# Performance work log

Measured on AMD Instinct MI355X. Metric: run time of the kernel, lower is better.

## Reference

```python
import jax, jax.numpy as jnp
import numpy as np

DIM = 1024
DIM_MEDIA = 1024
DIM_HEAD = 64
HEADS = 8
INNER = DIM_HEAD * HEADS  # 512
B, N_TOK, N_LAT = 4, 4096, 1024
LN_EPS = 1e-5


def setup_inputs() -> dict:
    key = jax.random.key(0)
    ks = jax.random.split(key, 6)
    x = jax.random.normal(ks[0], (B, N_TOK, DIM), dtype=jnp.float32)
    media = jax.random.normal(ks[1], (B, N_LAT, DIM_MEDIA), dtype=jnp.float32)
    media_mask = jax.random.randint(ks[2], (B, N_LAT), 0, 2).astype(bool)
    media_mask = media_mask.at[:, 0].set(True)  # avoid fully-masked rows (NaN softmax)
    ln_gamma = jnp.ones((DIM,), jnp.float32)
    ln_beta = jnp.zeros((DIM,), jnp.float32)
    Wq = jax.random.normal(ks[3], (DIM, INNER), jnp.float32) * (DIM ** -0.5)
    Wkv = jax.random.normal(ks[4], (DIM_MEDIA, 2 * INNER), jnp.float32) * (DIM_MEDIA ** -0.5)
    Wout = jax.random.normal(ks[5], (INNER, DIM), jnp.float32) * (INNER ** -0.5)
    return {"x": x, "media": media, "media_mask": media_mask,
            "ln_gamma": ln_gamma, "ln_beta": ln_beta,
            "Wq": Wq, "Wkv": Wkv, "Wout": Wout}


def reference(x, media, media_mask, ln_gamma, ln_beta, Wq, Wkv, Wout):
    scale = DIM_HEAD ** -0.5
    # LayerNorm over last dim
    mu = jnp.mean(x, axis=-1, keepdims=True)
    var = jnp.mean(jnp.square(x - mu), axis=-1, keepdims=True)
    xn = (x - mu) * jax.lax.rsqrt(var + LN_EPS) * ln_gamma + ln_beta

    q = (xn @ Wq) * scale                      # [b, n, inner]
    kv = media @ Wkv                           # [b, m, 2*inner]
    k, v = jnp.split(kv, 2, axis=-1)

    def to_heads(t):
        b, n, _ = t.shape
        return t.reshape(b, n, HEADS, DIM_HEAD).transpose(0, 2, 1, 3)  # b h n d

    q, k, v = to_heads(q), to_heads(k), to_heads(v)

    sim = jnp.einsum('bhid,bhjd->bhij', q, k)  # [b, h, n_tok, n_lat]
    neg_inf = jnp.float32(-jnp.inf)
    sim = jnp.where(media_mask[:, None, None, :], sim, neg_inf)
    sim = sim - jax.lax.stop_gradient(jnp.max(sim, axis=-1, keepdims=True))
    attn = jax.nn.softmax(sim, axis=-1)
    out = jnp.einsum('bhij,bhjd->bhid', attn, v)  # [b, h, n_tok, d]
    out = out.transpose(0, 2, 1, 3).reshape(out.shape[0], out.shape[2], INNER)
    return out @ Wout  # [b, n_tok, dim]
```

## Files before the change

### kernel.cpp

```cpp
#include <hip/hip_runtime.h>
#include <hip/hip_bf16.h>

typedef short bf16x8 __attribute__((ext_vector_type(8)));
typedef float f32x4 __attribute__((ext_vector_type(4)));
typedef unsigned short u16;

#define AS1 __attribute__((address_space(1)))
#define AS3 __attribute__((address_space(3)))

#define DIM     1024
#define INNER   512
#define HEADS   8
#define DHEAD   64
#define BATCH   4
#define NTOK    4096
#define NLAT    1024
#define M_X     (BATCH*NTOK)
#define M_MED   (BATCH*NLAT)
#define LN_EPS  1e-5f

__device__ __forceinline__ float b2f(u16 h) {
    union { unsigned u; float f; } v; v.u = ((unsigned)h) << 16; return v.f;
}
__device__ __forceinline__ u16 f2b(float f) {
    union { float f; unsigned u; } v; v.f = f;
    unsigned r = v.u + 0x7fff + ((v.u >> 16) & 1);
    return (u16)(r >> 16);
}

__launch_bounds__(256)
__global__ void detect_kernel(const unsigned* __restrict__ xw, const unsigned* __restrict__ maskw,
                              unsigned* __restrict__ flags) {
    __shared__ int s_bad, s_byte;
    if (threadIdx.x == 0) { s_bad = 0; s_byte = 0; }
    __syncthreads();
    unsigned w = xw[threadIdx.x];
    int bad = 0;
    #pragma unroll
    for (int h = 0; h < 2; h++) {
        unsigned el = (h ? (w >> 16) : w) & 0xFFFFu;
        unsigned ef = (el >> 7) & 0xFFu;
        if (!((ef >= 64u && ef < 192u) || (el & 0x7FFFu) == 0u)) bad = 1;
    }
    if (bad) atomicOr(&s_bad, 1);
    for (int i = threadIdx.x; i < NLAT; i += 256)
        if (maskw[i] > 1u) { atomicOr(&s_byte, 1); break; }
    __syncthreads();
    if (threadIdx.x == 0) { flags[0] = s_bad ? 0u : 1u; flags[1] = s_byte ? 1u : 0u; }
}

#define PREP_BLOCKS 8196

__device__ __forceinline__ void do_transpose(const void* in, u16* out, int R, int C,
                                             int bx, int by, bool bf, u16 (*t)[33]) {
    int c0 = bx * 32, r0 = by * 32;
    int tid = threadIdx.x;
    int r = tid >> 3, cb = (tid & 7) * 4;
    size_t base = (size_t)(r0 + r) * C + c0 + cb;
    u16 e0, e1, e2, e3;
    if (bf) {
        ushort4 a = *(const ushort4*)((const u16*)in + base);
        e0 = a.x; e1 = a.y; e2 = a.z; e3 = a.w;
    } else {
        float4 a = *(const float4*)((const float*)in + base);
        e0 = f2b(a.x); e1 = f2b(a.y); e2 = f2b(a.z); e3 = f2b(a.w);
    }
    t[r][cb] = e0; t[r][cb + 1] = e1; t[r][cb + 2] = e2; t[r][cb + 3] = e3;
    __syncthreads();
    ushort4 o;
    o.x = t[cb + 0][r]; o.y = t[cb + 1][r]; o.z = t[cb + 2][r]; o.w = t[cb + 3][r];
    *(ushort4*)(out + (size_t)(c0 + r) * R + r0 + cb) = o;
}

__launch_bounds__(256)
__global__ void prep_kernel(const void* __restrict__ x, const void* __restrict__ g,
                            const void* __restrict__ bt, u16* __restrict__ xn,
                            const void* __restrict__ media, u16* __restrict__ media_c,
                            const void* __restrict__ mask, int* __restrict__ map,
                            int* __restrict__ cnt,
                            const void* __restrict__ Wq, u16* __restrict__ WqT,
                            const void* __restrict__ Wkv, u16* __restrict__ WkvT,
                            const void* __restrict__ Wout, u16* __restrict__ WoutT,
                            const unsigned* __restrict__ flags) {
    __shared__ int wsumI[4];
    __shared__ u16 t[32][33];
    bool bf = flags[0] != 0;
    int bid = blockIdx.x, tid = threadIdx.x;

    if (bid < 4096) {
        int w = tid >> 6, lane = tid & 63;
        int row = (bid << 2) + w;
        float v[16];
        if (bf) {
            const u16* xr = (const u16*)x + (size_t)row * DIM;
            #pragma unroll
            for (int i = 0; i < 2; i++) {
                bf16x8 a = *(const bf16x8*)(xr + (size_t)(lane + 64 * i) * 8);
                #pragma unroll
                for (int j = 0; j < 8; j++) v[i * 8 + j] = b2f((u16)a[j]);
            }
        } else {
            const float* xr = (const float*)x + (size_t)row * DIM;
            #pragma unroll
            for (int i = 0; i < 4; i++) {
                float4 a = *(const float4*)(xr + (size_t)(lane + 64 * i) * 4);
                v[i * 4 + 0] = a.x; v[i * 4 + 1] = a.y;
                v[i * 4 + 2] = a.z; v[i * 4 + 3] = a.w;
            }
        }
        float s = 0.f, s2 = 0.f;
        #pragma unroll
        for (int i = 0; i < 16; i++) { s += v[i]; s2 += v[i] * v[i]; }
        #pragma unroll
        for (int m = 1; m < 64; m <<= 1) { s += __shfl_xor(s, m); s2 += __shfl_xor(s2, m); }
        float mu = s * (1.f / DIM);
        float var = s2 * (1.f / DIM) - mu * mu;
        float inv = rsqrtf(fmaxf(var, 0.f) + LN_EPS);
        u16* orow = xn + (size_t)row * DIM;
        if (bf) {
            const u16* gr = (const u16*)g;
            const u16* br = (const u16*)bt;
            #pragma unroll
            for (int i = 0; i < 2; i++) {
                int c = (lane + 64 * i) * 8;
                bf16x8 ga = *(const bf16x8*)(gr + c);
                bf16x8 ba = *(const bf16x8*)(br + c);
                u16 o[8];
                #pragma unroll
                for (int j = 0; j < 8; j++)
                    o[j] = f2b((v[i * 8 + j] - mu) * inv * b2f((u16)ga[j]) + b2f((u16)ba[j]));
                *(bf16x8*)(orow + c) = *(bf16x8*)o;
            }
        } else {
            const float* gr = (const float*)g;
            const float* br = (const float*)bt;
            #pragma unroll
            for (int i = 0; i < 4; i++) {
                int c = (lane + 64 * i) * 4;
                float4 ga = *(const float4*)(gr + c);
                float4 ba = *(const float4*)(br + c);
                ushort4 o;
                o.x = f2b((v[i * 4 + 0] - mu) * inv * ga.x + ba.x);
                o.y = f2b((v[i * 4 + 1] - mu) * inv * ga.y + ba.y);
                o.z = f2b((v[i * 4 + 2] - mu) * inv * ga.z + ba.z);
                o.w = f2b((v[i * 4 + 3] - mu) * inv * ga.w + ba.w);
                *(ushort4*)(orow + c) = o;
            }
        }
    } else if (bid < 6144) {
        size_t i = ((size_t)(bid - 4096) * 256 + tid) * 8;
        if (bf) {
            *(bf16x8*)(media_c + i) = *(const bf16x8*)((const u16*)media + i);
        } else {
            const float* s = (const float*)media + i;
            float4 a = *(const float4*)s, b = *(const float4*)(s + 4);
            u16 o[8] = {f2b(a.x), f2b(a.y), f2b(a.z), f2b(a.w),
                        f2b(b.x), f2b(b.y), f2b(b.z), f2b(b.w)};
            *(bf16x8*)(media_c + i) = *(bf16x8*)o;
        }
    } else if (bid < 6148) {
        int b = bid - 6144;
        bool bytes = flags[1] != 0;
        int v[4];
        if (bytes) {
            unsigned wd = ((const unsigned*)mask)[b * 256 + tid];
            #pragma unroll
            for (int i = 0; i < 4; i++) v[i] = ((wd >> (8 * i)) & 0xFFu) ? 1 : 0;
        } else {
            int4 m4 = ((const int4*)mask)[b * 256 + tid];
            v[0] = m4.x != 0; v[1] = m4.y != 0; v[2] = m4.z != 0; v[3] = m4.w != 0;
        }
        int tsum = v[0] + v[1] + v[2] + v[3];
        int lane = tid & 63, w = tid >> 6;
        int incl = tsum;
        #pragma unroll
        for (int off = 1; off < 64; off <<= 1) {
            int tt = __shfl_up(incl, off);
            if (lane >= off) incl += tt;
        }
        if (lane == 63) wsumI[w] = incl;
        __syncthreads();
        int base = 0;
        for (int k = 0; k < w; k++) base += wsumI[k];
        int slot = base + incl - tsum;
        int gbase = b * NLAT + tid * 4;
        #pragma unroll
        for (int i = 0; i < 4; i++) map[gbase + i] = v[i] ? slot++ : -1;
        if (tid == 0) cnt[b] = wsumI[0] + wsumI[1] + wsumI[2] + wsumI[3];
    } else if (bid < 6660) {
        int idx = bid - 6148;
        do_transpose(Wq, WqT, DIM, INNER, idx & 15, idx >> 4, bf, t);
    } else if (bid < 7684) {
        int idx = bid - 6660;
        do_transpose(Wkv, WkvT, DIM, DIM, idx & 31, idx >> 5, bf, t);
    } else {
        int idx = bid - 7684;
        do_transpose(Wout, WoutT, INNER, DIM, idx & 31, idx >> 5, bf, t);
    }
}

__launch_bounds__(256, 2)
__global__ void gemm128(const u16* __restrict__ A, const u16* __restrict__ Bt,
                        u16* __restrict__ C, float* __restrict__ Cf, int Ndim, int K,
                        float scale, int mode, u16* __restrict__ vT,
                        const int* __restrict__ map,
                        const unsigned* __restrict__ flags) {
    __shared__ __align__(16) u16 As[128 * 32];
    __shared__ __align__(16) u16 Bs[128 * 32];
    bool outbf = (mode != 2) || (flags[0] != 0);
    int n0 = blockIdx.x * 128, m0 = blockIdx.y * 128;
    int tid = threadIdx.x;
    int w = tid >> 6, lane = tid & 63, quad = lane >> 4, l15 = lane & 15;
    int wm = (w >> 1) * 64, wn = (w & 1) * 64;
    f32x4 acc[4][4] = {};
    int rowInSeg = lane >> 2;
    int colB = (((lane & 3) ^ ((lane >> 3) & 3))) * 8;
    for (int k0 = 0; k0 < K; k0 += 32) {
        __syncthreads();
        #pragma unroll
        for (int i = 0; i < 2; i++) {
            int seg = w * 2 + i;
            int row = seg * 16 + rowInSeg;
            __builtin_amdgcn_global_load_lds(
                (const AS1 void*)(A + (size_t)(m0 + row) * K + k0 + colB),
                (AS3 void*)(As + seg * 512), 16, 0, 0);
            __builtin_amdgcn_global_load_lds(
                (const AS1 void*)(Bt + (size_t)(n0 + row) * K + k0 + colB),
                (AS3 void*)(Bs + seg * 512), 16, 0, 0);
        }
        __syncthreads();
        int sw = quad ^ ((l15 >> 1) & 3);
        bf16x8 af[4], bfr[4];
        #pragma unroll
        for (int i = 0; i < 4; i++)
            af[i] = *(bf16x8*)&As[(wm + i * 16 + l15) * 32 + sw * 8];
        #pragma unroll
        for (int j = 0; j < 4; j++)
            bfr[j] = *(bf16x8*)&Bs[(wn + j * 16 + l15) * 32 + sw * 8];
        #pragma unroll
        for (int i = 0; i < 4; i++)
            #pragma unroll
            for (int j = 0; j < 4; j++)
                acc[i][j] = __builtin_amdgcn_mfma_f32_16x16x32_bf16(af[i], bfr[j], acc[i][j], 0, 0, 0);
    }
    #pragma unroll
    for (int i = 0; i < 4; i++)
        #pragma unroll
        for (int j = 0; j < 4; j++)
            #pragma unroll
            for (int r = 0; r < 4; r++) {
                int row = m0 + wm + i * 16 + quad * 4 + r;
                int col = n0 + wn + j * 16 + l15;
                float val = acc[i][j][r] * scale;
                if (mode == 1) {
                    int b = row >> 10, jj = row & 1023;
                    int slot = map[(b << 10) + jj];
                    if (slot >= 0) {
                        if (col < INNER) {
                            C[((size_t)(b << 10) + slot) * INNER + col] = f2b(val);
                        } else {
                            int c = col - INNER;
                            int h = c >> 6, d = c & 63;
                            vT[(((size_t)(b * HEADS + h) * 64 + d) << 10) + slot] = f2b(val);
                        }
                    }
                } else if (outbf) {
                    C[(size_t)row * Ndim + col] = f2b(val);
                } else {
                    Cf[(size_t)row * Ndim + col] = val;
                }
            }
}

__launch_bounds__(256, 6)
__global__ void flash_kernel(const u16* __restrict__ q, const u16* __restrict__ Kc,
                             const u16* __restrict__ vTc, const int* __restrict__ cntp,
                             u16* __restrict__ attn_out) {
    __shared__ __align__(16) u16 Ks[64 * 64];
    __shared__ __align__(16) u16 Vts[64 * 64];
    __shared__ __align__(16) u16 Ps[4][16 * 68];
    int bh = blockIdx.x >> 6;
    int qt = blockIdx.x & 63;
    int b = bh >> 3, h = bh & 7;
    int tid = threadIdx.x, w = tid >> 6, lane = tid & 63, quad = lane >> 4, l15 = lane & 15;
    int qrow0 = qt * 64 + w * 16;
    int cnt = cntp[b];

    size_t qbase = ((size_t)(b * NTOK) + qrow0 + l15) * INNER + h * 64;
    bf16x8 qf[2];
    qf[0] = *(const bf16x8*)(q + qbase + quad * 8);
    qf[1] = *(const bf16x8*)(q + qbase + 32 + quad * 8);

    f32x4 Oacc[4] = {};
    float lsum[4] = {0.f, 0.f, 0.f, 0.f};
    int ld_row = lane >> 3;
    int ld_col = ((lane & 7) ^ ld_row) * 8;

    for (int jt = 0; jt < cnt; jt += 64) {
        __syncthreads();
        #pragma unroll
        for (int i = 0; i < 2; i++) {
            int seg = w * 2 + i;
            int j = jt + seg * 8 + ld_row;
            __builtin_amdgcn_global_load_lds(
                (const AS1 void*)(Kc + ((size_t)(b * NLAT) + j) * INNER + h * 64 + ld_col),
                (AS3 void*)(Ks + seg * 512), 16, 0, 0);
            int d = seg * 8 + ld_row;
            __builtin_amdgcn_global_load_lds(
                (const AS1 void*)(vTc + (((size_t)(b * HEADS + h) * 64 + d) << 10) + jt + ld_col),
                (AS3 void*)(Vts + seg * 512), 16, 0, 0);
        }
        __syncthreads();

        int sw0 = (quad ^ (l15 & 7)) * 8;
        int sw1 = ((quad + 4) ^ (l15 & 7)) * 8;
        f32x4 S[4];
        #pragma unroll
        for (int c = 0; c < 4; c++) {
            bf16x8 kf0 = *(bf16x8*)&Ks[(c * 16 + l15) * 64 + sw0];
            bf16x8 kf1 = *(bf16x8*)&Ks[(c * 16 + l15) * 64 + sw1];
            f32x4 s = {};
            s = __builtin_amdgcn_mfma_f32_16x16x32_bf16(qf[0], kf0, s, 0, 0, 0);
            s = __builtin_amdgcn_mfma_f32_16x16x32_bf16(qf[1], kf1, s, 0, 0, 0);
            S[c] = s;
        }
        #pragma unroll
        for (int c = 0; c < 4; c++) {
            bool valid = (jt + c * 16 + l15) < cnt;
            #pragma unroll
            for (int r = 0; r < 4; r++) {
                float p = valid ? __expf(fminf(S[c][r], 80.f)) : 0.f;
                lsum[r] += p;
                Ps[w][(quad * 4 + r) * 68 + c * 16 + l15] = f2b(p);
            }
        }
        asm volatile("s_waitcnt lgkmcnt(0)" ::: "memory");
        bf16x8 pf0 = *(bf16x8*)&Ps[w][l15 * 68 + quad * 8];
        bf16x8 pf1 = *(bf16x8*)&Ps[w][l15 * 68 + 32 + quad * 8];
        #pragma unroll
        for (int dt = 0; dt < 4; dt++) {
            bf16x8 vf0 = *(bf16x8*)&Vts[(dt * 16 + l15) * 64 + sw0];
            bf16x8 vf1 = *(bf16x8*)&Vts[(dt * 16 + l15) * 64 + sw1];
            Oacc[dt] = __builtin_amdgcn_mfma_f32_16x16x32_bf16(pf0, vf0, Oacc[dt], 0, 0, 0);
            Oacc[dt] = __builtin_amdgcn_mfma_f32_16x16x32_bf16(pf1, vf1, Oacc[dt], 0, 0, 0);
        }
    }
    #pragma unroll
    for (int r = 0; r < 4; r++) {
        float l = lsum[r];
        l += __shfl_xor(l, 1);
        l += __shfl_xor(l, 2);
        l += __shfl_xor(l, 4);
        l += __shfl_xor(l, 8);
        float invl = (l > 0.f) ? (1.f / l) : 0.f;
        #pragma unroll
        for (int dt = 0; dt < 4; dt++) {
            int row = qrow0 + quad * 4 + r;
            int col = h * 64 + dt * 16 + l15;
            attn_out[(size_t)(b * NTOK + row) * INNER + col] = f2b(Oacc[dt][r] * invl);
        }
    }
}

extern "C" void kernel_launch(void* const* d_in, const int* in_sizes, int n_in,
                              void* d_out, int out_size, void* d_ws, size_t ws_size,
                              hipStream_t stream) {
    const void* x     = d_in[0];
    const void* media = d_in[1];
    const void* mask  = d_in[2];
    const void* g     = d_in[3];
    const void* beta  = d_in[4];
    const void* Wq    = d_in[5];
    const void* Wkv   = d_in[6];
    const void* Wout  = d_in[7];

    char* ws = (char*)d_ws;
    unsigned* flags = (unsigned*)ws;   ws += 256;
    int* map_c  = (int*)ws;            ws += (size_t)M_MED * 4;
    int* cnt_c  = (int*)ws;            ws += 256;
    u16* media_c = (u16*)ws;           ws += (size_t)M_MED * DIM * 2;
    u16* xn    = (u16*)ws;             ws += (size_t)M_X * DIM * 2;
    u16* qb    = (u16*)ws;             ws += (size_t)M_X * INNER * 2;
    u16* Kb    = (u16*)ws;             ws += (size_t)M_MED * INNER * 2;
    u16* vTb   = (u16*)ws;             ws += (size_t)M_MED * INNER * 2;
    u16* ao    = (u16*)ws;             ws += (size_t)M_X * INNER * 2;
    u16* WqT   = (u16*)ws;             ws += (size_t)DIM * INNER * 2;
    u16* WkvT  = (u16*)ws;             ws += (size_t)DIM * DIM * 2;
    u16* WoutT = (u16*)ws;             ws += (size_t)INNER * DIM * 2;

    detect_kernel<<<1, 256, 0, stream>>>((const unsigned*)x, (const unsigned*)mask, flags);
    prep_kernel<<<PREP_BLOCKS, 256, 0, stream>>>(x, g, beta, xn, media, media_c, mask, map_c, cnt_c,
                                                 Wq, WqT, Wkv, WkvT, Wout, WoutT, flags);
    gemm128<<<dim3(INNER / 128, M_X / 128), 256, 0, stream>>>(xn, WqT, qb, (float*)nullptr, INNER, DIM,
                                                              0.125f, 0, (u16*)nullptr, (int*)nullptr, flags);
    gemm128<<<dim3(DIM / 128, M_MED / 128), 256, 0, stream>>>(media_c, WkvT, Kb, (float*)nullptr, DIM, DIM,
                                                              1.0f, 1, vTb, map_c, flags);
    flash_kernel<<<dim3(32 * 64), 256, 0, stream>>>(qb, Kb, vTb, cnt_c, ao);
    gemm128<<<dim3(DIM / 128, M_X / 128), 256, 0, stream>>>(ao, WoutT, (u16*)d_out, (float*)d_out, DIM, INNER,
                                                            1.0f, 2, (u16*)nullptr, (int*)nullptr, flags);
}
```

Measured before the change: 288.7 us.

## Double-buffer LDS tiles in GEMM and flash attention kernels

Both the GEMM and the flash attention kernel now keep two LDS buffers and issue the global-to-LDS load for the next K/V or K-slice tile before computing on the current one. This removes one barrier per iteration and lets memory latency overlap the MFMA work. In exchange LDS use per block doubles and the launch bounds change (GEMM from 2 to 3 blocks per CU, flash from 6 to 3), which alters occupancy. In the flash kernel the Ps writes and the final vmcnt wait now share iterations with in-flight prefetches.

```diff
diff --git a/kernel.cpp b/kernel.cpp
--- a/kernel.cpp
+++ b/kernel.cpp
@@ -199,14 +199,14 @@
     }
 }
 
-__launch_bounds__(256, 2)
+__launch_bounds__(256, 3)
 __global__ void gemm128(const u16* __restrict__ A, const u16* __restrict__ Bt,
                         u16* __restrict__ C, float* __restrict__ Cf, int Ndim, int K,
                         float scale, int mode, u16* __restrict__ vT,
                         const int* __restrict__ map,
                         const unsigned* __restrict__ flags) {
-    __shared__ __align__(16) u16 As[128 * 32];
-    __shared__ __align__(16) u16 Bs[128 * 32];
+    __shared__ __align__(16) u16 As[2][128 * 32];
+    __shared__ __align__(16) u16 Bs[2][128 * 32];
     bool outbf = (mode != 2) || (flags[0] != 0);
     int n0 = blockIdx.x * 128, m0 = blockIdx.y * 128;
     int tid = threadIdx.x;
@@ -215,33 +215,44 @@
     f32x4 acc[4][4] = {};
     int rowInSeg = lane >> 2;
     int colB = (((lane & 3) ^ ((lane >> 3) & 3))) * 8;
-    for (int k0 = 0; k0 < K; k0 += 32) {
-        __syncthreads();
+    int sw = quad ^ ((l15 >> 1) & 3);
+
+    auto STAGE = [&](int buf, int k0) {
         #pragma unroll
         for (int i = 0; i < 2; i++) {
             int seg = w * 2 + i;
             int row = seg * 16 + rowInSeg;
             __builtin_amdgcn_global_load_lds(
                 (const AS1 void*)(A + (size_t)(m0 + row) * K + k0 + colB),
-                (AS3 void*)(As + seg * 512), 16, 0, 0);
+                (AS3 void*)(&As[buf][seg * 512]), 16, 0, 0);
             __builtin_amdgcn_global_load_lds(
                 (const AS1 void*)(Bt + (size_t)(n0 + row) * K + k0 + colB),
-                (AS3 void*)(Bs + seg * 512), 16, 0, 0);
-        }
-        __syncthreads();
-        int sw = quad ^ ((l15 >> 1) & 3);
+                (AS3 void*)(&Bs[buf][seg * 512]), 16, 0, 0);
+        }
+    };
+
+    int nt = K >> 5;
+    STAGE(0, 0);
+    asm volatile("s_waitcnt vmcnt(0)" ::: "memory");
+    __syncthreads();
+    int cur = 0;
+    for (int t = 0; t < nt; ++t) {
+        if (t + 1 < nt) STAGE(cur ^ 1, (t + 1) << 5);
         bf16x8 af[4], bfr[4];
         #pragma unroll
         for (int i = 0; i < 4; i++)
-            af[i] = *(bf16x8*)&As[(wm + i * 16 + l15) * 32 + sw * 8];
+            af[i] = *(bf16x8*)&As[cur][(wm + i * 16 + l15) * 32 + sw * 8];
         #pragma unroll
         for (int j = 0; j < 4; j++)
-            bfr[j] = *(bf16x8*)&Bs[(wn + j * 16 + l15) * 32 + sw * 8];
+            bfr[j] = *(bf16x8*)&Bs[cur][(wn + j * 16 + l15) * 32 + sw * 8];
         #pragma unroll
         for (int i = 0; i < 4; i++)
             #pragma unroll
             for (int j = 0; j < 4; j++)
                 acc[i][j] = __builtin_amdgcn_mfma_f32_16x16x32_bf16(af[i], bfr[j], acc[i][j], 0, 0, 0);
+        asm volatile("s_waitcnt vmcnt(0)" ::: "memory");
+        __syncthreads();
+        cur ^= 1;
     }
     #pragma unroll
     for (int i = 0; i < 4; i++)
@@ -272,12 +283,12 @@
             }
 }
 
-__launch_bounds__(256, 6)
+__launch_bounds__(256, 3)
 __global__ void flash_kernel(const u16* __restrict__ q, const u16* __restrict__ Kc,
                              const u16* __restrict__ vTc, const int* __restrict__ cntp,
                              u16* __restrict__ attn_out) {
-    __shared__ __align__(16) u16 Ks[64 * 64];
-    __shared__ __align__(16) u16 Vts[64 * 64];
+    __shared__ __align__(16) u16 Ks[2][64 * 64];
+    __shared__ __align__(16) u16 Vts[2][64 * 64];
     __shared__ __align__(16) u16 Ps[4][16 * 68];
     int bh = blockIdx.x >> 6;
     int qt = blockIdx.x & 63;
@@ -296,29 +307,36 @@
     int ld_row = lane >> 3;
     int ld_col = ((lane & 7) ^ ld_row) * 8;
 
-    for (int jt = 0; jt < cnt; jt += 64) {
-        __syncthreads();
+    auto STAGE = [&](int buf, int jt) {
         #pragma unroll
         for (int i = 0; i < 2; i++) {
             int seg = w * 2 + i;
             int j = jt + seg * 8 + ld_row;
             __builtin_amdgcn_global_load_lds(
                 (const AS1 void*)(Kc + ((size_t)(b * NLAT) + j) * INNER + h * 64 + ld_col),
-                (AS3 void*)(Ks + seg * 512), 16, 0, 0);
+                (AS3 void*)(&Ks[buf][seg * 512]), 16, 0, 0);
             int d = seg * 8 + ld_row;
             __builtin_amdgcn_global_load_lds(
                 (const AS1 void*)(vTc + (((size_t)(b * HEADS + h) * 64 + d) << 10) + jt + ld_col),
-                (AS3 void*)(Vts + seg * 512), 16, 0, 0);
-        }
-        __syncthreads();
+                (AS3 void*)(&Vts[buf][seg * 512]), 16, 0, 0);
+        }
+    };
+
+    STAGE(0, 0);
+    asm volatile("s_waitcnt vmcnt(0)" ::: "memory");
+    __syncthreads();
+    int cur = 0;
+
+    for (int jt = 0; jt < cnt; jt += 64) {
+        if (jt + 64 < cnt) STAGE(cur ^ 1, jt + 64);
 
         int sw0 = (quad ^ (l15 & 7)) * 8;
         int sw1 = ((quad + 4) ^ (l15 & 7)) * 8;
         f32x4 S[4];
         #pragma unroll
         for (int c = 0; c < 4; c++) {
-            bf16x8 kf0 = *(bf16x8*)&Ks[(c * 16 + l15) * 64 + sw0];
-            bf16x8 kf1 = *(bf16x8*)&Ks[(c * 16 + l15) * 64 + sw1];
+            bf16x8 kf0 = *(bf16x8*)&Ks[cur][(c * 16 + l15) * 64 + sw0];
+            bf16x8 kf1 = *(bf16x8*)&Ks[cur][(c * 16 + l15) * 64 + sw1];
             f32x4 s = {};
             s = __builtin_amdgcn_mfma_f32_16x16x32_bf16(qf[0], kf0, s, 0, 0, 0);
             s = __builtin_amdgcn_mfma_f32_16x16x32_bf16(qf[1], kf1, s, 0, 0, 0);
@@ -339,11 +357,14 @@
         bf16x8 pf1 = *(bf16x8*)&Ps[w][l15 * 68 + 32 + quad * 8];
         #pragma unroll
         for (int dt = 0; dt < 4; dt++) {
-            bf16x8 vf0 = *(bf16x8*)&Vts[(dt * 16 + l15) * 64 + sw0];
-            bf16x8 vf1 = *(bf16x8*)&Vts[(dt * 16 + l15) * 64 + sw1];
+            bf16x8 vf0 = *(bf16x8*)&Vts[cur][(dt * 16 + l15) * 64 + sw0];
+            bf16x8 vf1 = *(bf16x8*)&Vts[cur][(dt * 16 + l15) * 64 + sw1];
             Oacc[dt] = __builtin_amdgcn_mfma_f32_16x16x32_bf16(pf0, vf0, Oacc[dt], 0, 0, 0);
             Oacc[dt] = __builtin_amdgcn_mfma_f32_16x16x32_bf16(pf1, vf1, Oacc[dt], 0, 0, 0);
         }
+        asm volatile("s_waitcnt vmcnt(0)" ::: "memory");
+        __syncthreads();
+        cur ^= 1;
     }
     #pragma unroll
     for (int r = 0; r < 4; r++) {
```

Measured after the change: 294.3 us. Within noise of the previous version (+2.0%).

## Fold log2e into Q scale, transpose score MFMA, pack bf16 P stores, two-row LayerNorm

Applied to the files above, without the earlier changes.

The Q projection scale now includes log2(e), so the flash kernel can use exp2f in place of __expf. The QK^T MFMA operands are swapped so each lane holds one query row's scores. That lets P be packed with v_cvt_pk_bf16_f32 into 8-byte LDS stores and the row sum be kept in a single register. Full KV tiles skip the per-element mask check, and the prep LayerNorm handles two rows per wave with fewer blocks. The main risk is the transposed score layout and the lane-shuffle reduction, which must stay consistent with the P·V read pattern.

```diff
diff --git a/kernel.cpp b/kernel.cpp
--- a/kernel.cpp
+++ b/kernel.cpp
@@ -26,6 +26,11 @@
     union { float f; unsigned u; } v; v.f = f;
     unsigned r = v.u + 0x7fff + ((v.u >> 16) & 1);
     return (u16)(r >> 16);
+}
+__device__ __forceinline__ unsigned cvt_pk(float lo, float hi) {
+    unsigned r;
+    asm("v_cvt_pk_bf16_f32 %0, %1, %2" : "=v"(r) : "v"(lo), "v"(hi));
+    return r;
 }
 
 __launch_bounds__(256)
@@ -49,7 +54,7 @@
     if (threadIdx.x == 0) { flags[0] = s_bad ? 0u : 1u; flags[1] = s_byte ? 1u : 0u; }
 }
 
-#define PREP_BLOCKS 8196
+#define PREP_BLOCKS 6148
 
 __device__ __forceinline__ void do_transpose(const void* in, u16* out, int R, int C,
                                              int bx, int by, bool bf, u16 (*t)[33]) {
@@ -87,36 +92,62 @@
     bool bf = flags[0] != 0;
     int bid = blockIdx.x, tid = threadIdx.x;
 
-    if (bid < 4096) {
+    if (bid < 2048) {
         int w = tid >> 6, lane = tid & 63;
-        int row = (bid << 2) + w;
-        float v[16];
+        int row0 = (bid << 3) + (w << 1);
+        float v[2][16];
         if (bf) {
-            const u16* xr = (const u16*)x + (size_t)row * DIM;
-            #pragma unroll
-            for (int i = 0; i < 2; i++) {
-                bf16x8 a = *(const bf16x8*)(xr + (size_t)(lane + 64 * i) * 8);
-                #pragma unroll
-                for (int j = 0; j < 8; j++) v[i * 8 + j] = b2f((u16)a[j]);
-            }
+            const u16* xr = (const u16*)x + (size_t)row0 * DIM;
+            bf16x8 a[4];
+            #pragma unroll
+            for (int rr = 0; rr < 2; rr++)
+                #pragma unroll
+                for (int i = 0; i < 2; i++)
+                    a[rr * 2 + i] = *(const bf16x8*)(xr + (size_t)rr * DIM + (lane + 64 * i) * 8);
+            #pragma unroll
+            for (int rr = 0; rr < 2; rr++)
+                #pragma unroll
+                for (int i = 0; i < 2; i++)
+                    #pragma unroll
+                    for (int j = 0; j < 8; j++)
+                        v[rr][i * 8 + j] = b2f((u16)a[rr * 2 + i][j]);
         } else {
-            const float* xr = (const float*)x + (size_t)row * DIM;
-            #pragma unroll
-            for (int i = 0; i < 4; i++) {
-                float4 a = *(const float4*)(xr + (size_t)(lane + 64 * i) * 4);
-                v[i * 4 + 0] = a.x; v[i * 4 + 1] = a.y;
-                v[i * 4 + 2] = a.z; v[i * 4 + 3] = a.w;
-            }
-        }
-        float s = 0.f, s2 = 0.f;
-        #pragma unroll
-        for (int i = 0; i < 16; i++) { s += v[i]; s2 += v[i] * v[i]; }
-        #pragma unroll
-        for (int m = 1; m < 64; m <<= 1) { s += __shfl_xor(s, m); s2 += __shfl_xor(s2, m); }
-        float mu = s * (1.f / DIM);
-        float var = s2 * (1.f / DIM) - mu * mu;
-        float inv = rsqrtf(fmaxf(var, 0.f) + LN_EPS);
-        u16* orow = xn + (size_t)row * DIM;
+            const float* xr = (const float*)x + (size_t)row0 * DIM;
+            float4 a[8];
+            #pragma unroll
+            for (int rr = 0; rr < 2; rr++)
+                #pragma unroll
+                for (int i = 0; i < 4; i++)
+                    a[rr * 4 + i] = *(const float4*)(xr + (size_t)rr * DIM + (lane + 64 * i) * 4);
+            #pragma unroll
+            for (int rr = 0; rr < 2; rr++)
+                #pragma unroll
+                for (int i = 0; i < 4; i++) {
+                    v[rr][i * 4 + 0] = a[rr * 4 + i].x; v[rr][i * 4 + 1] = a[rr * 4 + i].y;
+                    v[rr][i * 4 + 2] = a[rr * 4 + i].z; v[rr][i * 4 + 3] = a[rr * 4 + i].w;
+                }
+        }
+        float s[2] = {0.f, 0.f}, s2[2] = {0.f, 0.f};
+        #pragma unroll
+        for (int rr = 0; rr < 2; rr++)
+            #pragma unroll
+            for (int i = 0; i < 16; i++) { s[rr] += v[rr][i]; s2[rr] += v[rr][i] * v[rr][i]; }
+        #pragma unroll
+        for (int m = 1; m < 64; m <<= 1) {
+            #pragma unroll
+            for (int rr = 0; rr < 2; rr++) {
+                s[rr] += __shfl_xor(s[rr], m);
+                s2[rr] += __shfl_xor(s2[rr], m);
+            }
+        }
+        float mu[2], inv[2];
+        #pragma unroll
+        for (int rr = 0; rr < 2; rr++) {
+            mu[rr] = s[rr] * (1.f / DIM);
+            float var = s2[rr] * (1.f / DIM) - mu[rr] * mu[rr];
+            inv[rr] = rsqrtf(fmaxf(var, 0.f) + LN_EPS);
+        }
+        u16* orow = xn + (size_t)row0 * DIM;
         if (bf) {
             const u16* gr = (const u16*)g;
             const u16* br = (const u16*)bt;
@@ -125,11 +156,14 @@
                 int c = (lane + 64 * i) * 8;
                 bf16x8 ga = *(const bf16x8*)(gr + c);
                 bf16x8 ba = *(const bf16x8*)(br + c);
-                u16 o[8];
-                #pragma unroll
-                for (int j = 0; j < 8; j++)
-                    o[j] = f2b((v[i * 8 + j] - mu) * inv * b2f((u16)ga[j]) + b2f((u16)ba[j]));
-                *(bf16x8*)(orow + c) = *(bf16x8*)o;
+                #pragma unroll
+                for (int rr = 0; rr < 2; rr++) {
+                    u16 o[8];
+                    #pragma unroll
+                    for (int j = 0; j < 8; j++)
+                        o[j] = f2b((v[rr][i * 8 + j] - mu[rr]) * inv[rr] * b2f((u16)ga[j]) + b2f((u16)ba[j]));
+                    *(bf16x8*)(orow + (size_t)rr * DIM + c) = *(bf16x8*)o;
+                }
             }
         } else {
             const float* gr = (const float*)g;
@@ -139,16 +173,19 @@
                 int c = (lane + 64 * i) * 4;
                 float4 ga = *(const float4*)(gr + c);
                 float4 ba = *(const float4*)(br + c);
-                ushort4 o;
-                o.x = f2b((v[i * 4 + 0] - mu) * inv * ga.x + ba.x);
-                o.y = f2b((v[i * 4 + 1] - mu) * inv * ga.y + ba.y);
-                o.z = f2b((v[i * 4 + 2] - mu) * inv * ga.z + ba.z);
-                o.w = f2b((v[i * 4 + 3] - mu) * inv * ga.w + ba.w);
-                *(ushort4*)(orow + c) = o;
-            }
-        }
-    } else if (bid < 6144) {
-        size_t i = ((size_t)(bid - 4096) * 256 + tid) * 8;
+                #pragma unroll
+                for (int rr = 0; rr < 2; rr++) {
+                    ushort4 o;
+                    o.x = f2b((v[rr][i * 4 + 0] - mu[rr]) * inv[rr] * ga.x + ba.x);
+                    o.y = f2b((v[rr][i * 4 + 1] - mu[rr]) * inv[rr] * ga.y + ba.y);
+                    o.z = f2b((v[rr][i * 4 + 2] - mu[rr]) * inv[rr] * ga.z + ba.z);
+                    o.w = f2b((v[rr][i * 4 + 3] - mu[rr]) * inv[rr] * ga.w + ba.w);
+                    *(ushort4*)(orow + (size_t)rr * DIM + c) = o;
+                }
+            }
+        }
+    } else if (bid < 4096) {
+        size_t i = ((size_t)(bid - 2048) * 256 + tid) * 8;
         if (bf) {
             *(bf16x8*)(media_c + i) = *(const bf16x8*)((const u16*)media + i);
         } else {
@@ -158,8 +195,8 @@
                         f2b(b.x), f2b(b.y), f2b(b.z), f2b(b.w)};
             *(bf16x8*)(media_c + i) = *(bf16x8*)o;
         }
-    } else if (bid < 6148) {
-        int b = bid - 6144;
+    } else if (bid < 4100) {
+        int b = bid - 4096;
         bool bytes = flags[1] != 0;
         int v[4];
         if (bytes) {
@@ -187,14 +224,14 @@
         #pragma unroll
         for (int i = 0; i < 4; i++) map[gbase + i] = v[i] ? slot++ : -1;
         if (tid == 0) cnt[b] = wsumI[0] + wsumI[1] + wsumI[2] + wsumI[3];
-    } else if (bid < 6660) {
-        int idx = bid - 6148;
+    } else if (bid < 4612) {
+        int idx = bid - 4100;
         do_transpose(Wq, WqT, DIM, INNER, idx & 15, idx >> 4, bf, t);
-    } else if (bid < 7684) {
-        int idx = bid - 6660;
+    } else if (bid < 5636) {
+        int idx = bid - 4612;
         do_transpose(Wkv, WkvT, DIM, DIM, idx & 31, idx >> 5, bf, t);
     } else {
-        int idx = bid - 7684;
+        int idx = bid - 5636;
         do_transpose(Wout, WoutT, INNER, DIM, idx & 31, idx >> 5, bf, t);
     }
 }
@@ -292,7 +329,7 @@
     qf[1] = *(const bf16x8*)(q + qbase + 32 + quad * 8);
 
     f32x4 Oacc[4] = {};
-    float lsum[4] = {0.f, 0.f, 0.f, 0.f};
+    float lsum = 0.f;
     int ld_row = lane >> 3;
     int ld_col = ((lane & 7) ^ ld_row) * 8;
 
@@ -320,18 +357,34 @@
             bf16x8 kf0 = *(bf16x8*)&Ks[(c * 16 + l15) * 64 + sw0];
             bf16x8 kf1 = *(bf16x8*)&Ks[(c * 16 + l15) * 64 + sw1];
             f32x4 s = {};
-            s = __builtin_amdgcn_mfma_f32_16x16x32_bf16(qf[0], kf0, s, 0, 0, 0);
-            s = __builtin_amdgcn_mfma_f32_16x16x32_bf16(qf[1], kf1, s, 0, 0, 0);
+            s = __builtin_amdgcn_mfma_f32_16x16x32_bf16(kf0, qf[0], s, 0, 0, 0);
+            s = __builtin_amdgcn_mfma_f32_16x16x32_bf16(kf1, qf[1], s, 0, 0, 0);
             S[c] = s;
         }
-        #pragma unroll
-        for (int c = 0; c < 4; c++) {
-            bool valid = (jt + c * 16 + l15) < cnt;
-            #pragma unroll
-            for (int r = 0; r < 4; r++) {
-                float p = valid ? __expf(fminf(S[c][r], 80.f)) : 0.f;
-                lsum[r] += p;
-                Ps[w][(quad * 4 + r) * 68 + c * 16 + l15] = f2b(p);
+        if (jt + 64 <= cnt) {
+            #pragma unroll
+            for (int c = 0; c < 4; c++) {
+                float p0 = exp2f(fminf(S[c][0], 115.4f));
+                float p1 = exp2f(fminf(S[c][1], 115.4f));
+                float p2 = exp2f(fminf(S[c][2], 115.4f));
+                float p3 = exp2f(fminf(S[c][3], 115.4f));
+                lsum += (p0 + p1) + (p2 + p3);
+                uint2 pw = {cvt_pk(p0, p1), cvt_pk(p2, p3)};
+                *(uint2*)&Ps[w][l15 * 68 + c * 16 + quad * 4] = pw;
+            }
+        } else {
+            #pragma unroll
+            for (int c = 0; c < 4; c++) {
+                int kbase = jt + c * 16 + quad * 4;
+                float p[4];
+                #pragma unroll
+                for (int r = 0; r < 4; r++) {
+                    bool valid = (kbase + r) < cnt;
+                    p[r] = valid ? exp2f(fminf(S[c][r], 115.4f)) : 0.f;
+                    lsum += p[r];
+                }
+                uint2 pw = {cvt_pk(p[0], p[1]), cvt_pk(p[2], p[3])};
+                *(uint2*)&Ps[w][l15 * 68 + c * 16 + quad * 4] = pw;
             }
         }
         asm volatile("s_waitcnt lgkmcnt(0)" ::: "memory");
@@ -345,13 +398,11 @@
             Oacc[dt] = __builtin_amdgcn_mfma_f32_16x16x32_bf16(pf1, vf1, Oacc[dt], 0, 0, 0);
         }
     }
+    lsum += __shfl_xor(lsum, 16);
+    lsum += __shfl_xor(lsum, 32);
     #pragma unroll
     for (int r = 0; r < 4; r++) {
-        float l = lsum[r];
-        l += __shfl_xor(l, 1);
-        l += __shfl_xor(l, 2);
-        l += __shfl_xor(l, 4);
-        l += __shfl_xor(l, 8);
+        float l = __shfl(lsum, quad * 4 + r);
         float invl = (l > 0.f) ? (1.f / l) : 0.f;
         #pragma unroll
         for (int dt = 0; dt < 4; dt++) {
@@ -392,7 +443,7 @@
     prep_kernel<<<PREP_BLOCKS, 256, 0, stream>>>(x, g, beta, xn, media, media_c, mask, map_c, cnt_c,
                                                  Wq, WqT, Wkv, WkvT, Wout, WoutT, flags);
     gemm128<<<dim3(INNER / 128, M_X / 128), 256, 0, stream>>>(xn, WqT, qb, (float*)nullptr, INNER, DIM,
-                                                              0.125f, 0, (u16*)nullptr, (int*)nullptr, flags);
+                                                              0.125f * 1.44269504f, 0, (u16*)nullptr, (int*)nullptr, flags);
     gemm128<<<dim3(DIM / 128, M_MED / 128), 256, 0, stream>>>(media_c, WkvT, Kb, (float*)nullptr, DIM, DIM,
                                                               1.0f, 1, vTb, map_c, flags);
     flash_kernel<<<dim3(32 * 64), 256, 0, stream>>>(qb, Kb, vTb, cnt_c, ao);
```

After: 291.0 us. Within noise of the previous version (+0.8%).
